# Kernel optimization log

Hardware: AMD Instinct MI355X
Metric: run time of the kernel (lower is better)

## Reference

```python
import jax, jax.numpy as jnp
import numpy as np

IN_DIM, HID, MID, FFN, OUT = 384, 128, 1024, 512, 1024
B, T = 8, 4096
LN_EPS = 1e-5


def _legs_hippo(n: int) -> np.ndarray:
    # A[i, j] = P_i(2j/n - 1) * sqrt(2i + 1), Legendre via 3-term recurrence
    x = 2.0 * np.arange(n) / n - 1.0          # eval points, shape [n]
    P = np.zeros((n, n), dtype=np.float64)     # P[i] = P_i(x)
    P[0] = 1.0
    if n > 1:
        P[1] = x
    for i in range(1, n - 1):
        P[i + 1] = ((2 * i + 1) * x * P[i] - i * P[i - 1]) / (i + 1)
    A = P * np.sqrt(2.0 * np.arange(n) + 1.0)[:, None]
    # rescale so the 4096-step recurrence stays finite (A is a free Parameter,
    # so any test value is valid; unscaled LegS overflows fp32 in ~20 steps)
    s = np.linalg.norm(A, 2)
    return (A / (1.05 * s)).astype(np.float32)


def _layernorm(x, g, b):
    mu = jnp.mean(x, axis=-1, keepdims=True)
    var = jnp.var(x, axis=-1, keepdims=True)
    return (x - mu) * jax.lax.rsqrt(var + LN_EPS) * g + b


def setup_inputs() -> dict:
    key = jax.random.key(0)
    ks = jax.random.split(key, 16)

    def w(k, shape, fan_in):
        return jax.random.normal(k, shape, jnp.float32) * (1.0 / np.sqrt(fan_in))

    return {
        "padded_x": jax.random.normal(ks[0], (B, T, IN_DIM), jnp.float32),
        "seq_lens": jax.random.randint(ks[1], (B,), 1, T + 1, jnp.int32),
        "A": jnp.asarray(_legs_hippo(HID)),
        "enc_w1": w(ks[2], (IN_DIM, MID), IN_DIM), "enc_b1": jnp.zeros((MID,), jnp.float32),
        "enc_w2": w(ks[3], (MID, HID), MID), "enc_b2": jnp.zeros((HID,), jnp.float32),
        "proj_w": w(ks[4], (HID, MID), HID), "proj_b": jnp.zeros((MID,), jnp.float32),
        "ln1_g": jnp.ones((MID,), jnp.float32), "ln1_b": jnp.zeros((MID,), jnp.float32),
        "ffn_w1": w(ks[5], (MID, FFN), MID), "ffn_b1": jnp.zeros((FFN,), jnp.float32),
        "ffn_w2": w(ks[6], (FFN, OUT), FFN), "ffn_b2": jnp.zeros((OUT,), jnp.float32),
        "ln2_g": jnp.ones((OUT,), jnp.float32), "ln2_b": jnp.zeros((OUT,), jnp.float32),
        "out_w": w(ks[7], (OUT, OUT), OUT), "out_b": jnp.zeros((OUT,), jnp.float32),
    }


def reference(padded_x, seq_lens, A, enc_w1, enc_b1, enc_w2, enc_b2,
              proj_w, proj_b, ln1_g, ln1_b, ffn_w1, ffn_b1, ffn_w2, ffn_b2,
              ln2_g, ln2_b, out_w, out_b):
    # encoder: Linear -> GELU(exact) -> Linear   [B, T, HID]
    h_mid = jax.nn.gelu(padded_x @ enc_w1 + enc_b1, approximate=False)
    seqs_bx = h_mid @ enc_w2 + enc_b2

    # masked linear recurrence h_t = A @ h_{t-1} + Bx_t via lax.scan over time
    xs = jnp.swapaxes(seqs_bx, 0, 1)           # [T, B, HID]
    ts = jnp.arange(xs.shape[0])

    def step(h, inp):
        x_t, t = inp
        upd = h @ A.T + x_t                     # (A @ h)^T batched
        mask = (t < seq_lens)[:, None]          # [B, 1]
        return jnp.where(mask, upd, h), None

    h0 = jnp.zeros((padded_x.shape[0], A.shape[0]), padded_x.dtype)
    batch_h, _ = jax.lax.scan(step, h0, (xs, ts))

    # decoder
    projected = batch_h @ proj_w + proj_b
    norm_h = _layernorm(projected, ln1_g, ln1_b)
    ffn_out = jax.nn.gelu(norm_h @ ffn_w1 + ffn_b1, approximate=False) @ ffn_w2 + ffn_b2
    ffn_out = ffn_out + projected               # residual (requires OUT == MID)
    norm_ffn = _layernorm(ffn_out, ln2_g, ln2_b)
    return norm_ffn @ out_w + out_b             # [B, OUT]
```

## Files before the change

### kernel.cpp

```cpp
#include <hip/hip_runtime.h>

typedef __attribute__((ext_vector_type(8))) short short8;
typedef __attribute__((ext_vector_type(4))) short short4v;
typedef __attribute__((ext_vector_type(4))) float float4v;

__device__ __forceinline__ float bf2f(short s) {
  union { float f; unsigned u; } cv; cv.u = ((unsigned)(unsigned short)s) << 16; return cv.f;
}
__device__ __forceinline__ short f2bf(float f) {
  union { float f; unsigned u; } cv; cv.f = f;
  unsigned u = cv.u;
  unsigned r = u + 0x7FFFu + ((u >> 16) & 1u);
  return (short)(r >> 16);
}
__device__ __forceinline__ float gelu_f(float v) {
  return 0.5f * v * (1.0f + erff(v * 0.70710678118654752440f));
}

template<int A_FP32, int EPI>
__global__ __launch_bounds__(256) void gemm_bt(
    const void* __restrict__ A_, const short* __restrict__ BT,
    const float* __restrict__ bias, void* __restrict__ out,
    int lda, int ldb, int ldc, int kSteps, int kChunk,
    const int* __restrict__ seq_lens, int seqSkip)
{
  int m0 = blockIdx.y * 128;
  int n0 = blockIdx.x * 128;
  if (seqSkip) {
    int b = m0 >> 12, t = m0 & 4095;
    if (t >= seq_lens[b]) return;
  }
  int kBase = blockIdx.z * kChunk;

  __shared__ short As[128 * 32];
  __shared__ short Bs[128 * 32];

  int tid = threadIdx.x;
  int lane = tid & 63, wave = tid >> 6;
  int l15 = lane & 15, quad = lane >> 4;
  int wm = wave & 1, wn = wave >> 1;

  float4v acc[4][4];
#pragma unroll
  for (int i = 0; i < 4; i++)
#pragma unroll
    for (int j = 0; j < 4; j++) acc[i][j] = 0;

  int r = tid >> 1;
  int off = (tid & 1) * 16;

  for (int ks = 0; ks < kSteps; ++ks) {
    int kk = kBase + ks * 32;
    if (A_FP32) {
      const float* Af = (const float*)A_ + (size_t)(m0 + r) * lda + kk + off;
      float4v x0 = ((const float4v*)Af)[0];
      float4v x1 = ((const float4v*)Af)[1];
      float4v x2 = ((const float4v*)Af)[2];
      float4v x3 = ((const float4v*)Af)[3];
      short tmp[16];
#pragma unroll
      for (int j = 0; j < 4; j++) {
        tmp[j] = f2bf(x0[j]); tmp[4 + j] = f2bf(x1[j]);
        tmp[8 + j] = f2bf(x2[j]); tmp[12 + j] = f2bf(x3[j]);
      }
      *(short8*)&As[r * 32 + off] = *(short8*)tmp;
      *(short8*)&As[r * 32 + off + 8] = *(short8*)(tmp + 8);
    } else {
      const short* Ab = (const short*)A_ + (size_t)(m0 + r) * lda + kk + off;
      *(short8*)&As[r * 32 + off]     = ((const short8*)Ab)[0];
      *(short8*)&As[r * 32 + off + 8] = ((const short8*)Ab)[1];
    }
    {
      const short* Bb = BT + (size_t)(n0 + r) * ldb + kk + off;
      *(short8*)&Bs[r * 32 + off]     = ((const short8*)Bb)[0];
      *(short8*)&Bs[r * 32 + off + 8] = ((const short8*)Bb)[1];
    }
    __syncthreads();
    short8 af[4], bfr[4];
#pragma unroll
    for (int im = 0; im < 4; im++)
      af[im] = *(short8*)&As[(wm * 64 + im * 16 + l15) * 32 + quad * 8];
#pragma unroll
    for (int in = 0; in < 4; in++)
      bfr[in] = *(short8*)&Bs[(wn * 64 + in * 16 + l15) * 32 + quad * 8];
#pragma unroll
    for (int im = 0; im < 4; im++)
#pragma unroll
      for (int in = 0; in < 4; in++)
        acc[im][in] = __builtin_amdgcn_mfma_f32_16x16x32_bf16(af[im], bfr[in], acc[im][in], 0, 0, 0);
    __syncthreads();
  }

#pragma unroll
  for (int im = 0; im < 4; im++) {
#pragma unroll
    for (int in = 0; in < 4; in++) {
      int n = n0 + wn * 64 + in * 16 + l15;
#pragma unroll
      for (int reg = 0; reg < 4; reg++) {
        int m = m0 + wm * 64 + im * 16 + quad * 4 + reg;
        float v = acc[im][in][reg];
        if (EPI == 0) {
          v += bias[n]; v = gelu_f(v);
          ((short*)out)[(size_t)m * ldc + n] = f2bf(v);
        } else if (EPI == 1) {
          v += bias[n];
          ((short*)out)[(size_t)m * ldc + n] = f2bf(v);
        } else {
          atomicAdd((float*)out + (size_t)m * ldc + n, v);
        }
      }
    }
  }
}

__global__ void prep_wide(const float* __restrict__ w1, const float* __restrict__ w2,
                          const float* __restrict__ proj_w, const float* __restrict__ ffn_w1,
                          const float* __restrict__ ffn_w2, const float* __restrict__ out_w,
                          const float* __restrict__ A,
                          short* __restrict__ w1T, short* __restrict__ w2T,
                          short* __restrict__ projB, short* __restrict__ ffn1B,
                          short* __restrict__ ffn2B, short* __restrict__ outB,
                          short* __restrict__ P1, short* __restrict__ P1t,
                          short* __restrict__ P2t,
                          short* __restrict__ Spow, short* __restrict__ SpowT)
{
  int idx = blockIdx.x * 256 + threadIdx.x;
  if (idx < 393216) {
    int n = idx / 384, k = idx % 384;
    w1T[idx] = f2bf(w1[k * 1024 + n]);
    return;
  }
  idx -= 393216;
  if (idx < 131072) {
    int n = idx / 1024, k = idx % 1024;
    w2T[idx] = f2bf(w2[k * 128 + n]);
    return;
  }
  idx -= 131072;
  if (idx < 131072) { projB[idx] = f2bf(proj_w[idx]); return; }
  idx -= 131072;
  if (idx < 524288) { ffn1B[idx] = f2bf(ffn_w1[idx]); return; }
  idx -= 524288;
  if (idx < 524288) { ffn2B[idx] = f2bf(ffn_w2[idx]); return; }
  idx -= 524288;
  if (idx < 1048576) { outB[idx] = f2bf(out_w[idx]); return; }
  idx -= 1048576;
  if (idx < 16384) {
    int i = idx >> 7, j = idx & 127;
    short bidv = f2bf((i == j) ? 1.0f : 0.0f);
    P1[i * 8192 + 63 * 128 + j] = bidv;
    P1t[(63 * 128 + j) * 128 + i] = bidv;
    P2t[(63 * 128 + j) * 128 + i] = bidv;
    short ab = f2bf(A[idx]);
    Spow[idx] = ab;
    SpowT[(size_t)j * 128 + i] = ab;
  }
}

__global__ __launch_bounds__(256) void pow_chain(short* __restrict__ Spow,
                                                 short* __restrict__ SpowT)
{
  __shared__ short X[16384];
  __shared__ short XT[16384];
  int t = threadIdx.x;
  for (int i = t * 8; i < 16384; i += 2048) {
    *(short8*)&X[i]  = *(const short8*)&Spow[i];
    *(short8*)&XT[i] = *(const short8*)&SpowT[i];
  }
  __syncthreads();
  int lane = t & 63, wave = t >> 6, l15 = lane & 15, quad = lane >> 4;
  for (int step = 1; step <= 11; ++step) {
    short8 af[2][4], bfr[8][4];
#pragma unroll
    for (int mt = 0; mt < 2; mt++)
#pragma unroll
      for (int ks = 0; ks < 4; ks++)
        af[mt][ks] = *(short8*)&X[(wave * 32 + mt * 16 + l15) * 128 + ks * 32 + quad * 8];
#pragma unroll
    for (int nt = 0; nt < 8; nt++)
#pragma unroll
      for (int ks = 0; ks < 4; ks++)
        bfr[nt][ks] = *(short8*)&XT[(nt * 16 + l15) * 128 + ks * 32 + quad * 8];
    __syncthreads();
    float4v acc[2][8];
#pragma unroll
    for (int mt = 0; mt < 2; mt++)
#pragma unroll
      for (int nt = 0; nt < 8; nt++) acc[mt][nt] = 0;
#pragma unroll
    for (int ks = 0; ks < 4; ks++)
#pragma unroll
      for (int mt = 0; mt < 2; mt++)
#pragma unroll
        for (int nt = 0; nt < 8; nt++)
          acc[mt][nt] = __builtin_amdgcn_mfma_f32_16x16x32_bf16(af[mt][ks], bfr[nt][ks], acc[mt][nt], 0, 0, 0);
    short* gX  = Spow  + (size_t)step * 16384;
    short* gXT = SpowT + (size_t)step * 16384;
#pragma unroll
    for (int mt = 0; mt < 2; mt++)
#pragma unroll
      for (int nt = 0; nt < 8; nt++)
#pragma unroll
        for (int reg = 0; reg < 4; reg++) {
          int m = wave * 32 + mt * 16 + quad * 4 + reg;
          int n = nt * 16 + l15;
          short v = f2bf(acc[mt][nt][reg]);
          X[m * 128 + n] = v; XT[n * 128 + m] = v;
          gX[m * 128 + n] = v; gXT[n * 128 + m] = v;
        }
    __syncthreads();
  }
}

__global__ __launch_bounds__(256) void pow_fill(const short* __restrict__ Spow,
                                                const short* __restrict__ SpowT,
                                                short* __restrict__ P1,
                                                short* __restrict__ P1t,
                                                short* __restrict__ P2t)
{
  __shared__ short cur[16384];
  __shared__ short Bt[16384];
  int bid = blockIdx.x;
  int table1 = bid < 63;
  int e = table1 ? bid + 1 : bid - 62;
  int t = threadIdx.x;
  int lane = t & 63, wave = t >> 6, l15 = lane & 15, quad = lane >> 4;

  int bits = e;
  int k0 = __ffs(bits) - 1; bits &= bits - 1;
  int s0 = table1 ? k0 : (k0 == 0 ? 6 : 6 + k0);
  for (int i = t * 8; i < 16384; i += 2048)
    *(short8*)&cur[i] = *(const short8*)&Spow[(size_t)s0 * 16384 + i];

  while (bits) {
    int k = __ffs(bits) - 1; bits &= bits - 1;
    int si = table1 ? k : (k == 0 ? 6 : 6 + k);
    for (int i = t * 8; i < 16384; i += 2048)
      *(short8*)&Bt[i] = *(const short8*)&SpowT[(size_t)si * 16384 + i];
    __syncthreads();
    short8 af[2][4], bfr[8][4];
#pragma unroll
    for (int mt = 0; mt < 2; mt++)
#pragma unroll
      for (int ks = 0; ks < 4; ks++)
        af[mt][ks] = *(short8*)&cur[(wave * 32 + mt * 16 + l15) * 128 + ks * 32 + quad * 8];
#pragma unroll
    for (int nt = 0; nt < 8; nt++)
#pragma unroll
      for (int ks = 0; ks < 4; ks++)
        bfr[nt][ks] = *(short8*)&Bt[(nt * 16 + l15) * 128 + ks * 32 + quad * 8];
    __syncthreads();
    float4v acc[2][8];
#pragma unroll
    for (int mt = 0; mt < 2; mt++)
#pragma unroll
      for (int nt = 0; nt < 8; nt++) acc[mt][nt] = 0;
#pragma unroll
    for (int ks = 0; ks < 4; ks++)
#pragma unroll
      for (int mt = 0; mt < 2; mt++)
#pragma unroll
        for (int nt = 0; nt < 8; nt++)
          acc[mt][nt] = __builtin_amdgcn_mfma_f32_16x16x32_bf16(af[mt][ks], bfr[nt][ks], acc[mt][nt], 0, 0, 0);
#pragma unroll
    for (int mt = 0; mt < 2; mt++)
#pragma unroll
      for (int nt = 0; nt < 8; nt++)
#pragma unroll
        for (int reg = 0; reg < 4; reg++) {
          int m = wave * 32 + mt * 16 + quad * 4 + reg;
          int n = nt * 16 + l15;
          cur[m * 128 + n] = f2bf(acc[mt][nt][reg]);
        }
    __syncthreads();
  }
  __syncthreads();
  int slot = 63 - e;
  for (int idx = t; idx < 16384; idx += 256) {
    int i = idx >> 7, j = idx & 127;
    short v = cur[idx];
    if (table1) {
      P1[i * 8192 + slot * 128 + j] = v;
      P1t[(slot * 128 + j) * 128 + i] = v;
    } else {
      P2t[(slot * 128 + j) * 128 + i] = v;
    }
  }
}

__global__ void build_shift(const float* __restrict__ V, const short* __restrict__ seqs,
                            const int* __restrict__ seq_lens,
                            short* __restrict__ Vsh, short* __restrict__ TlX)
{
  int idx = blockIdx.x * 256 + threadIdx.x;
  int pp = idx >> 16;
  int e = idx & 65535;
  int k = e >> 3, b = e & 7;
  int cp = k >> 7, i = k & 127;
  int L = seq_lens[b];
  short v = 0;
  if (pp == 0) {
    int F = L >> 6;
    int sh = 64 - F;
    if (cp >= sh) v = f2bf(V[(size_t)(b * 64 + (cp - sh)) * 128 + i]);
    Vsh[e] = v;
  } else {
    int F = L >> 6, rr = L & 63;
    int sh = 64 - rr;
    if (cp >= sh) v = seqs[((size_t)b * 4096 + F * 64 + (cp - sh)) * 128 + i];
    TlX[e] = v;
  }
}

__global__ __launch_bounds__(256) void tiny_gemm(
    const short* __restrict__ Vsh, const short* __restrict__ TlX,
    const short* __restrict__ P2t, const short* __restrict__ P1t,
    float* __restrict__ hFtail)
{
  int pp = blockIdx.x >> 4, ks = blockIdx.x & 15;
  const short* X = pp ? TlX : Vsh;
  const short* P = pp ? P1t : P2t;
  float* outp = hFtail + pp * 1024;
  int i = threadIdx.x & 127, g = threadIdx.x >> 7;
  float acc[4] = {0, 0, 0, 0};
  for (int k = ks * 512; k < ks * 512 + 512; ++k) {
    float pv = bf2f(P[k * 128 + i]);
    short4v xv = *(const short4v*)(X + k * 8 + g * 4);
#pragma unroll
    for (int q = 0; q < 4; q++) acc[q] += bf2f(xv[q]) * pv;
  }
#pragma unroll
  for (int q = 0; q < 4; q++) atomicAdd(&outp[(g * 4 + q) * 128 + i], acc[q]);
}

__global__ __launch_bounds__(256) void proj_stage(
    const float* __restrict__ hFtail, const short* __restrict__ P1t,
    const int* __restrict__ seq_lens, const short* __restrict__ projB,
    const float* __restrict__ proj_b, float* __restrict__ projected)
{
  __shared__ short hT[128 * 8];
  __shared__ float red[4][64][8];
  int t = threadIdx.x;
  {
    int b = t >> 5, i4 = (t & 31) * 4;
    int rr = seq_lens[b] & 63;
    const short* M = P1t + (size_t)(63 - rr) * 128 * 128;
    const float* hF = hFtail + b * 128;
    float acc[4];
#pragma unroll
    for (int q = 0; q < 4; q++) acc[q] = hFtail[1024 + b * 128 + i4 + q];
    for (int j = 0; j < 128; ++j) {
      float hv = hF[j];
      short4v mv = *(const short4v*)&M[j * 128 + i4];
#pragma unroll
      for (int q = 0; q < 4; q++) acc[q] += bf2f(mv[q]) * hv;
    }
#pragma unroll
    for (int q = 0; q < 4; q++) hT[(i4 + q) * 8 + b] = f2bf(acc[q]);
  }
  __syncthreads();
  int c = t & 63, sl = t >> 6;
  int n = blockIdx.x * 64 + c;
  float acc[8] = {0, 0, 0, 0, 0, 0, 0, 0};
  for (int k = sl * 32; k < sl * 32 + 32; ++k) {
    short8 xv = *(short8*)&hT[k * 8];
    float wv = bf2f(projB[k * 1024 + n]);
#pragma unroll
    for (int b = 0; b < 8; b++) acc[b] += bf2f(xv[b]) * wv;
  }
#pragma unroll
  for (int b = 0; b < 8; b++) red[sl][c][b] = acc[b];
  __syncthreads();
  if (sl == 0) {
#pragma unroll
    for (int s = 1; s < 4; s++)
#pragma unroll
      for (int b = 0; b < 8; b++) acc[b] += red[s][c][b];
    float bn = proj_b[n];
#pragma unroll
    for (int b = 0; b < 8; b++) projected[b * 1024 + n] = acc[b] + bn;
  }
}

__global__ __launch_bounds__(256) void ffn1_stage(
    const float* __restrict__ projected, const float* __restrict__ g1,
    const float* __restrict__ b1, const short* __restrict__ ffn1B,
    float* __restrict__ ffn1raw)
{
  __shared__ float part[8][32][2];
  __shared__ float stats[8][2];
  __shared__ short xT[256 * 8];
  __shared__ float red[4][64][8];
  int t = threadIdx.x;
  { int b = t >> 5, j0 = t & 31; float s = 0, q = 0;
    for (int k = j0 * 32; k < j0 * 32 + 32; ++k) { float v = projected[b * 1024 + k]; s += v; q += v * v; }
    part[b][j0][0] = s; part[b][j0][1] = q; }
  __syncthreads();
  if (t < 8) {
    float s = 0, q = 0;
    for (int j = 0; j < 32; j++) { s += part[t][j][0]; q += part[t][j][1]; }
    float mu = s * (1.0f / 1024.0f);
    float var = q * (1.0f / 1024.0f) - mu * mu;
    stats[t][0] = mu; stats[t][1] = rsqrtf(var + 1e-5f);
  }
  __syncthreads();
  int ky0 = blockIdx.y * 256;
  for (int idx = t; idx < 2048; idx += 256) {
    int kl = idx >> 3, b = idx & 7; int k = ky0 + kl;
    float v = (projected[b * 1024 + k] - stats[b][0]) * stats[b][1] * g1[k] + b1[k];
    xT[kl * 8 + b] = f2bf(v);
  }
  __syncthreads();
  int c = t & 63, sl = t >> 6;
  int n = blockIdx.x * 64 + c;
  float acc[8] = {0, 0, 0, 0, 0, 0, 0, 0};
  for (int kl = sl * 64; kl < sl * 64 + 64; ++kl) {
    short8 xv = *(short8*)&xT[kl * 8];
    float wv = bf2f(ffn1B[(size_t)(ky0 + kl) * 512 + n]);
#pragma unroll
    for (int b = 0; b < 8; b++) acc[b] += bf2f(xv[b]) * wv;
  }
#pragma unroll
  for (int b = 0; b < 8; b++) red[sl][c][b] = acc[b];
  __syncthreads();
  if (sl == 0) {
#pragma unroll
    for (int s = 1; s < 4; s++)
#pragma unroll
      for (int b = 0; b < 8; b++) acc[b] += red[s][c][b];
#pragma unroll
    for (int b = 0; b < 8; b++) atomicAdd(&ffn1raw[b * 512 + n], acc[b]);
  }
}

__global__ __launch_bounds__(256) void ffn2_stage(
    const float* __restrict__ ffn1raw, const float* __restrict__ fb1,
    const short* __restrict__ ffn2B, float* __restrict__ ffn2raw)
{
  __shared__ short xT[256 * 8];
  __shared__ float red[4][64][8];
  int t = threadIdx.x;
  int ky0 = blockIdx.y * 256;
  for (int idx = t; idx < 2048; idx += 256) {
    int kl = idx >> 3, b = idx & 7; int k = ky0 + kl;
    float v = gelu_f(ffn1raw[b * 512 + k] + fb1[k]);
    xT[kl * 8 + b] = f2bf(v);
  }
  __syncthreads();
  int c = t & 63, sl = t >> 6;
  int n = blockIdx.x * 64 + c;
  float acc[8] = {0, 0, 0, 0, 0, 0, 0, 0};
  for (int kl = sl * 64; kl < sl * 64 + 64; ++kl) {
    short8 xv = *(short8*)&xT[kl * 8];
    float wv = bf2f(ffn2B[(size_t)(ky0 + kl) * 1024 + n]);
#pragma unroll
    for (int b = 0; b < 8; b++) acc[b] += bf2f(xv[b]) * wv;
  }
#pragma unroll
  for (int b = 0; b < 8; b++) red[sl][c][b] = acc[b];
  __syncthreads();
  if (sl == 0) {
#pragma unroll
    for (int s = 1; s < 4; s++)
#pragma unroll
      for (int b = 0; b < 8; b++) acc[b] += red[s][c][b];
#pragma unroll
    for (int b = 0; b < 8; b++) atomicAdd(&ffn2raw[b * 1024 + n], acc[b]);
  }
}

__global__ __launch_bounds__(256) void out_stage(
    const float* __restrict__ ffn2raw, const float* __restrict__ fb2,
    const float* __restrict__ projected, const float* __restrict__ g2,
    const float* __restrict__ b2ln, const short* __restrict__ outB,
    const float* __restrict__ out_b, float* __restrict__ d_out)
{
  __shared__ float part[8][32][2];
  __shared__ float stats[8][2];
  __shared__ short xT[512 * 8];
  __shared__ float red[4][64][8];
  int t = threadIdx.x;
  { int b = t >> 5, j0 = t & 31; float s = 0, q = 0;
    for (int k = j0 * 32; k < j0 * 32 + 32; ++k) {
      float v = ffn2raw[b * 1024 + k] + fb2[k] + projected[b * 1024 + k];
      s += v; q += v * v;
    }
    part[b][j0][0] = s; part[b][j0][1] = q; }
  __syncthreads();
  if (t < 8) {
    float s = 0, q = 0;
    for (int j = 0; j < 32; j++) { s += part[t][j][0]; q += part[t][j][1]; }
    float mu = s * (1.0f / 1024.0f);
    float var = q * (1.0f / 1024.0f) - mu * mu;
    stats[t][0] = mu; stats[t][1] = rsqrtf(var + 1e-5f);
  }
  __syncthreads();
  int ky0 = blockIdx.y * 512;
  for (int idx = t; idx < 4096; idx += 256) {
    int kl = idx >> 3, b = idx & 7; int k = ky0 + kl;
    float v = ffn2raw[b * 1024 + k] + fb2[k] + projected[b * 1024 + k];
    v = (v - stats[b][0]) * stats[b][1] * g2[k] + b2ln[k];
    xT[kl * 8 + b] = f2bf(v);
  }
  __syncthreads();
  int c = t & 63, sl = t >> 6;
  int n = blockIdx.x * 64 + c;
  float acc[8] = {0, 0, 0, 0, 0, 0, 0, 0};
  for (int kl = sl * 128; kl < sl * 128 + 128; ++kl) {
    short8 xv = *(short8*)&xT[kl * 8];
    float wv = bf2f(outB[(size_t)(ky0 + kl) * 1024 + n]);
#pragma unroll
    for (int b = 0; b < 8; b++) acc[b] += bf2f(xv[b]) * wv;
  }
#pragma unroll
  for (int b = 0; b < 8; b++) red[sl][c][b] = acc[b];
  __syncthreads();
  if (sl == 0) {
#pragma unroll
    for (int s = 1; s < 4; s++)
#pragma unroll
      for (int b = 0; b < 8; b++) acc[b] += red[s][c][b];
    float bn = (blockIdx.y == 0) ? out_b[n] : 0.0f;
#pragma unroll
    for (int b = 0; b < 8; b++) atomicAdd(&d_out[b * 1024 + n], acc[b] + bn);
  }
}

extern "C" void kernel_launch(void* const* d_in, const int* in_sizes, int n_in,
                              void* d_out, int out_size, void* d_ws, size_t ws_size,
                              hipStream_t stream)
{
  (void)in_sizes; (void)n_in; (void)out_size; (void)ws_size;
  const float* x      = (const float*)d_in[0];
  const int* seq_lens = (const int*)d_in[1];
  const float* A      = (const float*)d_in[2];
  const float* enc_w1 = (const float*)d_in[3];
  const float* enc_b1 = (const float*)d_in[4];
  const float* enc_w2 = (const float*)d_in[5];
  const float* enc_b2 = (const float*)d_in[6];
  const float* proj_w = (const float*)d_in[7];
  const float* proj_b = (const float*)d_in[8];
  const float* ln1_g  = (const float*)d_in[9];
  const float* ln1_b  = (const float*)d_in[10];
  const float* ffn_w1 = (const float*)d_in[11];
  const float* ffn_b1 = (const float*)d_in[12];
  const float* ffn_w2 = (const float*)d_in[13];
  const float* ffn_b2 = (const float*)d_in[14];
  const float* ln2_g  = (const float*)d_in[15];
  const float* ln2_b  = (const float*)d_in[16];
  const float* out_w  = (const float*)d_in[17];
  const float* out_b  = (const float*)d_in[18];

  char* p = (char*)d_ws;
  auto alloc = [&](size_t bytes) { char* r = p; p += (bytes + 255) & ~(size_t)255; return r; };
  short* h_mid = (short*)alloc(32768ull * 1024 * 2);
  short* seqs  = (short*)alloc(32768ull * 128 * 2);
  short* w1T   = (short*)alloc(1024ull * 384 * 2);
  short* w2T   = (short*)alloc(128ull * 1024 * 2);
  short* projB = (short*)alloc(128ull * 1024 * 2);
  short* ffn1B = (short*)alloc(1024ull * 512 * 2);
  short* ffn2B = (short*)alloc(512ull * 1024 * 2);
  short* outB  = (short*)alloc(1024ull * 1024 * 2);
  short* Spow  = (short*)alloc(12ull * 16384 * 2);
  short* SpowT = (short*)alloc(12ull * 16384 * 2);
  short* P1    = (short*)alloc(128ull * 8192 * 2);
  short* P1t   = (short*)alloc(8192ull * 128 * 2);
  short* P2t   = (short*)alloc(8192ull * 128 * 2);
  float* V       = (float*)alloc(512ull * 128 * 4);
  float* hFtail  = (float*)alloc(2ull * 8 * 128 * 4);
  float* ffn1raw = (float*)alloc(8ull * 512 * 4);
  float* ffn2raw = (float*)alloc(8ull * 1024 * 4);
  short* Vsh   = (short*)alloc(8192ull * 8 * 2);
  short* TlX   = (short*)alloc(8192ull * 8 * 2);
  float* projected = (float*)alloc(8ull * 1024 * 4);

  hipMemsetAsync(V, 0, (512ull * 128 + 2ull * 8 * 128 + 8ull * 512 + 8ull * 1024) * 4, stream);
  hipMemsetAsync(d_out, 0, 8192ull * 4, stream);

  prep_wide<<<10816, 256, 0, stream>>>(enc_w1, enc_w2, proj_w, ffn_w1, ffn_w2, out_w, A,
      w1T, w2T, projB, ffn1B, ffn2B, outB, P1, P1t, P2t, Spow, SpowT);
  pow_chain<<<1, 256, 0, stream>>>(Spow, SpowT);
  pow_fill<<<126, 256, 0, stream>>>(Spow, SpowT, P1, P1t, P2t);

  gemm_bt<1, 0><<<dim3(8, 256, 1), 256, 0, stream>>>(x, w1T, enc_b1, h_mid,
      384, 384, 1024, 12, 0, seq_lens, 1);
  gemm_bt<0, 1><<<dim3(1, 256, 1), 256, 0, stream>>>(h_mid, w2T, enc_b2, seqs,
      1024, 1024, 128, 32, 0, seq_lens, 1);

  gemm_bt<0, 2><<<dim3(1, 4, 16), 256, 0, stream>>>(seqs, P1, nullptr, V,
      8192, 8192, 128, 16, 512, seq_lens, 0);
  build_shift<<<512, 256, 0, stream>>>(V, seqs, seq_lens, Vsh, TlX);
  tiny_gemm<<<32, 256, 0, stream>>>(Vsh, TlX, P2t, P1t, hFtail);

  proj_stage<<<16, 256, 0, stream>>>(hFtail, P1t, seq_lens, projB, proj_b, projected);
  ffn1_stage<<<dim3(8, 4), 256, 0, stream>>>(projected, ln1_g, ln1_b, ffn1B, ffn1raw);
  ffn2_stage<<<dim3(16, 2), 256, 0, stream>>>(ffn1raw, ffn_b1, ffn2B, ffn2raw);
  out_stage<<<dim3(16, 2), 256, 0, stream>>>(ffn2raw, ffn_b2, projected, ln2_g, ln2_b,
      outB, out_b, (float*)d_out);
}
```

Before: 450.0 us.

## Use direct global-to-LDS loads with 64-wide K tiles and pre-convert input to bf16

The GEMM kernel now loads A and B tiles straight into shared memory with global_load_lds, so the data no longer passes through registers. The K tile doubles to 64, which halves the number of barrier pairs per K range. Because of this the fp32-A path is dropped, so the input x is converted to bf16 in a separate pass added to prep_wide. That pass costs an extra read and write of the whole 32768x384 input, even for rows the seq_lens skip would have ignored, and the kernel now has a larger LDS footprint.

```diff
diff --git a/kernel.cpp b/kernel.cpp
--- a/kernel.cpp
+++ b/kernel.cpp
@@ -16,10 +16,15 @@
 __device__ __forceinline__ float gelu_f(float v) {
   return 0.5f * v * (1.0f + erff(v * 0.70710678118654752440f));
 }
-
-template<int A_FP32, int EPI>
+__device__ __forceinline__ void glds16(const short* g, short* l) {
+  __builtin_amdgcn_global_load_lds(
+      (const __attribute__((address_space(1))) void*)g,
+      (__attribute__((address_space(3))) void*)l, 16, 0, 0);
+}
+
+template<int EPI>
 __global__ __launch_bounds__(256) void gemm_bt(
-    const void* __restrict__ A_, const short* __restrict__ BT,
+    const short* __restrict__ A_, const short* __restrict__ BT,
     const float* __restrict__ bias, void* __restrict__ out,
     int lda, int ldb, int ldc, int kSteps, int kChunk,
     const int* __restrict__ seq_lens, int seqSkip)
@@ -32,13 +37,14 @@
   }
   int kBase = blockIdx.z * kChunk;
 
-  __shared__ short As[128 * 32];
-  __shared__ short Bs[128 * 32];
+  __shared__ __align__(16) short As[128 * 64];
+  __shared__ __align__(16) short Bs[128 * 64];
 
   int tid = threadIdx.x;
   int lane = tid & 63, wave = tid >> 6;
   int l15 = lane & 15, quad = lane >> 4;
   int wm = wave & 1, wn = wave >> 1;
+  int lr = lane >> 3, lseg = lane & 7;
 
   float4v acc[4][4];
 #pragma unroll
@@ -46,48 +52,30 @@
 #pragma unroll
     for (int j = 0; j < 4; j++) acc[i][j] = 0;
 
-  int r = tid >> 1;
-  int off = (tid & 1) * 16;
-
   for (int ks = 0; ks < kSteps; ++ks) {
-    int kk = kBase + ks * 32;
-    if (A_FP32) {
-      const float* Af = (const float*)A_ + (size_t)(m0 + r) * lda + kk + off;
-      float4v x0 = ((const float4v*)Af)[0];
-      float4v x1 = ((const float4v*)Af)[1];
-      float4v x2 = ((const float4v*)Af)[2];
-      float4v x3 = ((const float4v*)Af)[3];
-      short tmp[16];
-#pragma unroll
-      for (int j = 0; j < 4; j++) {
-        tmp[j] = f2bf(x0[j]); tmp[4 + j] = f2bf(x1[j]);
-        tmp[8 + j] = f2bf(x2[j]); tmp[12 + j] = f2bf(x3[j]);
-      }
-      *(short8*)&As[r * 32 + off] = *(short8*)tmp;
-      *(short8*)&As[r * 32 + off + 8] = *(short8*)(tmp + 8);
-    } else {
-      const short* Ab = (const short*)A_ + (size_t)(m0 + r) * lda + kk + off;
-      *(short8*)&As[r * 32 + off]     = ((const short8*)Ab)[0];
-      *(short8*)&As[r * 32 + off + 8] = ((const short8*)Ab)[1];
-    }
-    {
-      const short* Bb = BT + (size_t)(n0 + r) * ldb + kk + off;
-      *(short8*)&Bs[r * 32 + off]     = ((const short8*)Bb)[0];
-      *(short8*)&Bs[r * 32 + off + 8] = ((const short8*)Bb)[1];
+    int kk = kBase + ks * 64;
+#pragma unroll
+    for (int i = 0; i < 4; i++) {
+      int rowg = wave * 32 + i * 8;
+      glds16(A_ + (size_t)(m0 + rowg + lr) * lda + kk + lseg * 8, &As[rowg * 64]);
+      glds16(BT + (size_t)(n0 + rowg + lr) * ldb + kk + lseg * 8, &Bs[rowg * 64]);
     }
     __syncthreads();
-    short8 af[4], bfr[4];
-#pragma unroll
-    for (int im = 0; im < 4; im++)
-      af[im] = *(short8*)&As[(wm * 64 + im * 16 + l15) * 32 + quad * 8];
-#pragma unroll
-    for (int in = 0; in < 4; in++)
-      bfr[in] = *(short8*)&Bs[(wn * 64 + in * 16 + l15) * 32 + quad * 8];
-#pragma unroll
-    for (int im = 0; im < 4; im++)
+#pragma unroll
+    for (int kh = 0; kh < 2; kh++) {
+      short8 af[4], bfr[4];
+#pragma unroll
+      for (int im = 0; im < 4; im++)
+        af[im] = *(short8*)&As[(wm * 64 + im * 16 + l15) * 64 + kh * 32 + quad * 8];
 #pragma unroll
       for (int in = 0; in < 4; in++)
-        acc[im][in] = __builtin_amdgcn_mfma_f32_16x16x32_bf16(af[im], bfr[in], acc[im][in], 0, 0, 0);
+        bfr[in] = *(short8*)&Bs[(wn * 64 + in * 16 + l15) * 64 + kh * 32 + quad * 8];
+#pragma unroll
+      for (int im = 0; im < 4; im++)
+#pragma unroll
+        for (int in = 0; in < 4; in++)
+          acc[im][in] = __builtin_amdgcn_mfma_f32_16x16x32_bf16(af[im], bfr[in], acc[im][in], 0, 0, 0);
+    }
     __syncthreads();
   }
 
@@ -114,10 +102,12 @@
   }
 }
 
-__global__ void prep_wide(const float* __restrict__ w1, const float* __restrict__ w2,
+__global__ void prep_wide(const float* __restrict__ x, const float* __restrict__ w1,
+                          const float* __restrict__ w2,
                           const float* __restrict__ proj_w, const float* __restrict__ ffn_w1,
                           const float* __restrict__ ffn_w2, const float* __restrict__ out_w,
                           const float* __restrict__ A,
+                          short* __restrict__ xB,
                           short* __restrict__ w1T, short* __restrict__ w2T,
                           short* __restrict__ projB, short* __restrict__ ffn1B,
                           short* __restrict__ ffn2B, short* __restrict__ outB,
@@ -126,6 +116,15 @@
                           short* __restrict__ Spow, short* __restrict__ SpowT)
 {
   int idx = blockIdx.x * 256 + threadIdx.x;
+  if (idx < 3145728) {
+    float4v v = ((const float4v*)x)[idx];
+    short4v o;
+#pragma unroll
+    for (int j = 0; j < 4; j++) o[j] = f2bf(v[j]);
+    ((short4v*)xB)[idx] = o;
+    return;
+  }
+  idx -= 3145728;
   if (idx < 393216) {
     int n = idx / 384, k = idx % 384;
     w1T[idx] = f2bf(w1[k * 1024 + n]);
@@ -555,6 +554,7 @@
   char* p = (char*)d_ws;
   auto alloc = [&](size_t bytes) { char* r = p; p += (bytes + 255) & ~(size_t)255; return r; };
   short* h_mid = (short*)alloc(32768ull * 1024 * 2);
+  short* xB    = (short*)alloc(32768ull * 384 * 2);
   short* seqs  = (short*)alloc(32768ull * 128 * 2);
   short* w1T   = (short*)alloc(1024ull * 384 * 2);
   short* w2T   = (short*)alloc(128ull * 1024 * 2);
@@ -578,18 +578,18 @@
   hipMemsetAsync(V, 0, (512ull * 128 + 2ull * 8 * 128 + 8ull * 512 + 8ull * 1024) * 4, stream);
   hipMemsetAsync(d_out, 0, 8192ull * 4, stream);
 
-  prep_wide<<<10816, 256, 0, stream>>>(enc_w1, enc_w2, proj_w, ffn_w1, ffn_w2, out_w, A,
-      w1T, w2T, projB, ffn1B, ffn2B, outB, P1, P1t, P2t, Spow, SpowT);
+  prep_wide<<<23104, 256, 0, stream>>>(x, enc_w1, enc_w2, proj_w, ffn_w1, ffn_w2, out_w, A,
+      xB, w1T, w2T, projB, ffn1B, ffn2B, outB, P1, P1t, P2t, Spow, SpowT);
   pow_chain<<<1, 256, 0, stream>>>(Spow, SpowT);
   pow_fill<<<126, 256, 0, stream>>>(Spow, SpowT, P1, P1t, P2t);
 
-  gemm_bt<1, 0><<<dim3(8, 256, 1), 256, 0, stream>>>(x, w1T, enc_b1, h_mid,
-      384, 384, 1024, 12, 0, seq_lens, 1);
-  gemm_bt<0, 1><<<dim3(1, 256, 1), 256, 0, stream>>>(h_mid, w2T, enc_b2, seqs,
-      1024, 1024, 128, 32, 0, seq_lens, 1);
-
-  gemm_bt<0, 2><<<dim3(1, 4, 16), 256, 0, stream>>>(seqs, P1, nullptr, V,
-      8192, 8192, 128, 16, 512, seq_lens, 0);
+  gemm_bt<0><<<dim3(8, 256, 1), 256, 0, stream>>>(xB, w1T, enc_b1, h_mid,
+      384, 384, 1024, 6, 0, seq_lens, 1);
+  gemm_bt<1><<<dim3(1, 256, 1), 256, 0, stream>>>(h_mid, w2T, enc_b2, seqs,
+      1024, 1024, 128, 16, 0, seq_lens, 1);
+
+  gemm_bt<2><<<dim3(1, 4, 16), 256, 0, stream>>>(seqs, P1, nullptr, V,
+      8192, 8192, 128, 8, 512, seq_lens, 0);
   build_shift<<<512, 256, 0, stream>>>(V, seqs, seq_lens, Vsh, TlX);
   tiny_gemm<<<32, 256, 0, stream>>>(Vsh, TlX, P2t, P1t, hFtail);
 
```

After: 441.1 us. 2.0% less time.
